# Performance work log

Measured on AMD Instinct MI355X. Metric: run time of the kernel, lower is better.

## Reference

```python
import jax, jax.numpy as jnp
import numpy as np

NALGOS = 64
NTASKS = 256
T = 4096  # len(lx)


def setup_inputs() -> dict:
    key = jax.random.key(0)
    ks = jax.random.split(key, 6)
    return {
        "lx": jax.random.randint(ks[0], (T,), 0, NTASKS),
        # task_matrix ~ U(-1, 1), as in the torch init
        "task_matrix": jax.random.uniform(ks[1], (NTASKS, NTASKS), jnp.float32) * 2.0 - 1.0,
        # task difficulty ~ U(0, 1); keep away from 0 to avoid division blowup
        "task_difficulty": jax.random.uniform(ks[2], (NTASKS,), jnp.float32, 0.05, 1.0),
        "alg_efficiency": 0.5 + 0.02 * jax.random.normal(ks[3], (NALGOS,), jnp.float32),
        "alg_memory_horizon": 0.5 + 0.1 * jax.random.normal(ks[4], (NALGOS,), jnp.float32),
        "alg_experience_boost": 0.5 + 0.02 * jax.random.normal(ks[5], (NALGOS,), jnp.float32),
    }


def reference(lx, task_matrix, task_difficulty, alg_efficiency,
              alg_memory_horizon, alg_experience_boost):
    # Faithful translation of IdealLearner.performance.
    # Original triple loop reads result[algo,task2,ind] and sig[algo,task,ind]
    # (previous timestep only) and writes index ind+1, so each timestep is
    # vectorizable over (algo, task2); only the time axis is a true recurrence.
    A = alg_efficiency.shape[0]
    N = task_matrix.shape[0]
    eff = alg_efficiency[:, None]        # (A,1)
    mem = alg_memory_horizon[:, None]    # (A,1)
    boost = alg_experience_boost[:, None]  # (A,1)
    diff = task_difficulty[None, :]      # (1,N) ; task_difficulty_scale == 1

    def step(carry, task):
        res_prev, sig_prev = carry              # each (A, N)
        tm = task_matrix[task][None, :]         # (1, N) row for current task
        sp = sig_prev[:, task][:, None]         # (A, 1) prior perf on current task
        res = res_prev * mem + tm * eff + tm * sp * boost
        sig = 2.0 * jax.nn.sigmoid(res / diff) - 1.0
        return (res, sig), sig

    z = jnp.zeros((A, N), task_matrix.dtype)
    _, ys = jax.lax.scan(step, (z, z), lx)      # ys: (T, A, N)
    # prepend the zero initial state -> (A, N, T+1), matching the torch output
    return jnp.concatenate([z[:, :, None], jnp.transpose(ys, (1, 2, 0))], axis=-1)
```

## Files before the change

kernel.cpp:

```cpp
#include <hip/hip_runtime.h>
#include <hip/hip_bf16.h>

#define NALGOS 64
#define NTASKS 256
#define TSTEPS 4096
#define CHUNK  256
#define NCHUNK (TSTEPS / CHUNK)
#define SUB    64
#define TP     257
#define LOG2E  1.44269504f

__global__ __launch_bounds__(64) void driver_kernel(
    const int* __restrict__ lx, const float* __restrict__ tmat,
    const float* __restrict__ diff, const float* __restrict__ eff_v,
    const float* __restrict__ mem_v, const float* __restrict__ boost_v,
    float* __restrict__ g_arr, float* __restrict__ ckpt) {
  __shared__ int    lx_s[TSTEPS + 8];
  __shared__ float  c_s[NTASKS];
  __shared__ float4 ctab[TSTEPS + 8];

  const int a = blockIdx.x;
  const int l = threadIdx.x;
  const float eff   = eff_v[a];
  const float mem   = mem_v[a];
  const float boost = boost_v[a];
  const float e0 = eff - boost;
  const float b2 = 2.0f * boost;

#pragma unroll 8
  for (int k = 0; k < TSTEPS / 64; ++k) lx_s[k * 64 + l] = lx[k * 64 + l];
  if (l < 8) lx_s[TSTEPS + l] = 0;
#pragma unroll
  for (int k = 0; k < NTASKS / 64; ++k) {
    float dk = diff[k * 64 + l];
    c_s[k * 64 + l] = -LOG2E / dk;
  }
  __syncthreads();

#pragma unroll 4
  for (int k = 0; k < TSTEPS / 64; ++k) {
    int i  = k * 64 + l;
    int t0 = lx_s[i];
    int t1 = (i + 1 < TSTEPS) ? lx_s[i + 1] : 0;
    int t2 = (i + 2 < TSTEPS) ? lx_s[i + 2] : 0;
    float q  = tmat[t0 * NTASKS + t1];
    float cp = c_s[t1];
    float4 e;
    e.x = cp;
    e.y = b2 * cp * q;
    e.z = e0 * cp * q;
    e.w = __int_as_float(t0 | (t2 << 16));
    ctab[i] = e;
  }
  if (l < 8) ctab[TSTEPS + l] = make_float4(0.f, 0.f, 0.f, __int_as_float(0));
  __syncthreads();

  const float4* rows = (const float4*)tmat;
  float* gout = g_arr + (size_t)a * TSTEPS;
  float* ck   = ckpt  + (size_t)a * NCHUNK * NTASKS;

  float r0 = 0.f, r1 = 0.f, r2 = 0.f, r3 = 0.f;
  float u = 2.0f;
  float keep_g = 0.f;

  float4 ct_cur = ctab[0];
  float4 ct_n1  = ctab[1];
  float4 ct_n2  = ctab[2];
  float  A = ct_cur.z;

  float4 tm0 = rows[lx_s[0] * 64 + l];
  float4 tm1 = rows[lx_s[1] * 64 + l];
  float4 tm2 = rows[lx_s[2] * 64 + l];
  float4 tm3 = rows[lx_s[3] * 64 + l];

#pragma unroll 4
  for (int t = 0; t < TSTEPS; ++t) {
    float w   = __builtin_amdgcn_rcpf(u);
    float g   = fmaf(b2, w, e0);
    float arg = fmaf(ct_cur.y, w, A);
    float ev  = __builtin_amdgcn_exp2f(arg);
    u = 1.0f + ev;

    keep_g = ((t & 63) == l) ? g : keep_g;

    r0 = fmaf(r0, mem, tm0.x * g);
    r1 = fmaf(r1, mem, tm0.y * g);
    r2 = fmaf(r2, mem, tm0.z * g);
    r3 = fmaf(r3, mem, tm0.w * g);

    int sb   = __float_as_int(ct_cur.w);
    int j2   = (sb >> 16) & 0xffff;
    int lane = j2 >> 2;
    float h01  = (j2 & 1) ? r1 : r0;
    float h23  = (j2 & 1) ? r3 : r2;
    float hsel = (j2 & 2) ? h23 : h01;
    float bro = __uint_as_float(
        __builtin_amdgcn_readlane(__float_as_uint(hsel), lane));
    float p = mem * bro;
    A = fmaf(ct_n1.x, p, ct_n1.z);

    ct_cur = ct_n1; ct_n1 = ct_n2; ct_n2 = ctab[t + 3];
    int nrow = lx_s[t + 4];
    tm0 = tm1; tm1 = tm2; tm2 = tm3;
    tm3 = rows[nrow * 64 + l];

    if ((t & 63) == 63) gout[t - 63 + l] = keep_g;
    if ((t & 255) == 255 && t < TSTEPS - 1) {
      float4 s; s.x = r0; s.y = r1; s.z = r2; s.w = r3;
      ((float4*)(ck + ((t + 1) >> 8) * NTASKS))[l] = s;
    }
  }
}

__global__ __launch_bounds__(256) void expand_kernel(
    const int* __restrict__ lx, const float* __restrict__ tmat,
    const float* __restrict__ diff, const float* __restrict__ mem_v,
    const float* __restrict__ g_arr, const float* __restrict__ ckpt,
    float* __restrict__ out) {
  __shared__ float tile[SUB * TP];
  __shared__ int   lx_c[CHUNK];
  __shared__ float g_c[CHUNK];

  const int c = blockIdx.x;
  const int a = blockIdx.y;
  const int n = threadIdx.x;

  const float mem = mem_v[a];
  const float cn  = -LOG2E / diff[n];
  float res = (c == 0) ? 0.f : ckpt[((size_t)a * NCHUNK + c) * NTASKS + n];

  const int t0 = c * CHUNK;
  lx_c[n] = lx[t0 + n];
  g_c[n]  = g_arr[(size_t)a * TSTEPS + t0 + n];
  __syncthreads();

  if (c == 0) out[((size_t)a * NTASKS + n) * (TSTEPS + 1)] = 0.f;

  const int tq   = threadIdx.x & 15;
  const int rloc = threadIdx.x >> 4;

  for (int tb = 0; tb < CHUNK; tb += SUB) {
#pragma unroll 8
    for (int ts = 0; ts < SUB; ++ts) {
      int   task = lx_c[tb + ts];
      float g    = g_c[tb + ts];
      float tm   = tmat[task * NTASKS + n];
      res = fmaf(res, mem, tm * g);
      float w = __builtin_amdgcn_rcpf(
          1.0f + __builtin_amdgcn_exp2f(cn * res));
      tile[ts * TP + n] = fmaf(2.0f, w, -1.0f);
    }
    __syncthreads();
    for (int rr = 0; rr < NTASKS; rr += 16) {
      const int row = rr + rloc;
      float v0 = tile[(4 * tq + 0) * TP + row];
      float v1 = tile[(4 * tq + 1) * TP + row];
      float v2 = tile[(4 * tq + 2) * TP + row];
      float v3 = tile[(4 * tq + 3) * TP + row];
      float4 v = make_float4(v0, v1, v2, v3);
      float* dst = &out[((size_t)a * NTASKS + row) * (TSTEPS + 1) +
                        t0 + tb + 4 * tq + 1];
      __builtin_memcpy(dst, &v, 16);
    }
    __syncthreads();
  }
}

extern "C" void kernel_launch(void* const* d_in, const int* in_sizes, int n_in,
                              void* d_out, int out_size, void* d_ws, size_t ws_size,
                              hipStream_t stream) {
  const int*   lx    = (const int*)d_in[0];
  const float* tmat  = (const float*)d_in[1];
  const float* diff  = (const float*)d_in[2];
  const float* eff   = (const float*)d_in[3];
  const float* mem   = (const float*)d_in[4];
  const float* boost = (const float*)d_in[5];
  float* out = (float*)d_out;

  float* g_arr = (float*)d_ws;
  float* ckpt  = g_arr + (size_t)NALGOS * TSTEPS;

  driver_kernel<<<NALGOS, 64, 0, stream>>>(lx, tmat, diff, eff, mem, boost,
                                           g_arr, ckpt);
  expand_kernel<<<dim3(NCHUNK, NALGOS), 256, 0, stream>>>(
      lx, tmat, diff, mem, g_arr, ckpt, out);
}
```

Before: 727.7 us.

## Deepen driver prefetch pipeline with register rings and remap expand grid

The driver kernel's serial recurrence loop now works in 64-step groups with a fully unrolled 32-step inner loop. It keeps a 4-deep ring of step coefficients and an 8-deep ring of task-matrix rows in registers, so row loads are issued 8 steps ahead instead of 4. The packed lane index and prefetch row are made wave-uniform via readfirstlane, and the per-step modulo checks for g and checkpoint stores are hoisted out to group boundaries. The expand kernel moves to a 1D grid with a custom block-to-(chunk, algo) mapping, probably to change how output writes are spread across memory channels. The cost is more registers held in the driver and a larger unrolled loop body.

```diff
diff --git a/kernel.cpp b/kernel.cpp
--- a/kernel.cpp
+++ b/kernel.cpp
@@ -15,7 +15,7 @@
     const float* __restrict__ diff, const float* __restrict__ eff_v,
     const float* __restrict__ mem_v, const float* __restrict__ boost_v,
     float* __restrict__ g_arr, float* __restrict__ ckpt) {
-  __shared__ int    lx_s[TSTEPS + 8];
+  __shared__ int    lx_s[TSTEPS + 16];
   __shared__ float  c_s[NTASKS];
   __shared__ float4 ctab[TSTEPS + 8];
 
@@ -29,7 +29,7 @@
 
 #pragma unroll 8
   for (int k = 0; k < TSTEPS / 64; ++k) lx_s[k * 64 + l] = lx[k * 64 + l];
-  if (l < 8) lx_s[TSTEPS + l] = 0;
+  if (l < 16) lx_s[TSTEPS + l] = 0;
 #pragma unroll
   for (int k = 0; k < NTASKS / 64; ++k) {
     float dk = diff[k * 64 + l];
@@ -41,15 +41,14 @@
   for (int k = 0; k < TSTEPS / 64; ++k) {
     int i  = k * 64 + l;
     int t0 = lx_s[i];
-    int t1 = (i + 1 < TSTEPS) ? lx_s[i + 1] : 0;
-    int t2 = (i + 2 < TSTEPS) ? lx_s[i + 2] : 0;
+    int t1 = lx_s[i + 1];
     float q  = tmat[t0 * NTASKS + t1];
     float cp = c_s[t1];
     float4 e;
     e.x = cp;
     e.y = b2 * cp * q;
     e.z = e0 * cp * q;
-    e.w = __int_as_float(t0 | (t2 << 16));
+    e.w = __int_as_float(lx_s[i + 2] | (lx_s[i + 8] << 16));
     ctab[i] = e;
   }
   if (l < 8) ctab[TSTEPS + l] = make_float4(0.f, 0.f, 0.f, __int_as_float(0));
@@ -63,51 +62,59 @@
   float u = 2.0f;
   float keep_g = 0.f;
 
-  float4 ct_cur = ctab[0];
-  float4 ct_n1  = ctab[1];
-  float4 ct_n2  = ctab[2];
-  float  A = ct_cur.z;
+  float4 ctr[4];
+  float4 tmr[8];
+#pragma unroll
+  for (int k = 0; k < 4; ++k) ctr[k] = ctab[k];
+#pragma unroll
+  for (int k = 0; k < 8; ++k) tmr[k] = rows[lx_s[k] * 64 + l];
+  float A = ctr[0].z;
 
-  float4 tm0 = rows[lx_s[0] * 64 + l];
-  float4 tm1 = rows[lx_s[1] * 64 + l];
-  float4 tm2 = rows[lx_s[2] * 64 + l];
-  float4 tm3 = rows[lx_s[3] * 64 + l];
+  for (int grp = 0; grp < TSTEPS / 64; ++grp) {
+#pragma unroll 1
+    for (int k32 = 0; k32 < 2; ++k32) {
+      const float4* cb = ctab + grp * 64 + k32 * 32;
+      const int kb = k32 * 32;
+#pragma unroll
+      for (int kk = 0; kk < 32; ++kk) {
+        const int k = kb + kk;
+        const float4 ct  = ctr[k & 3];
+        const float4 ctn = ctr[(k + 1) & 3];
+        const float4 tm  = tmr[k & 7];
 
-#pragma unroll 4
-  for (int t = 0; t < TSTEPS; ++t) {
-    float w   = __builtin_amdgcn_rcpf(u);
-    float g   = fmaf(b2, w, e0);
-    float arg = fmaf(ct_cur.y, w, A);
-    float ev  = __builtin_amdgcn_exp2f(arg);
-    u = 1.0f + ev;
+        float w   = __builtin_amdgcn_rcpf(u);
+        float gt  = fmaf(b2, w, e0);
+        float arg = fmaf(ct.y, w, A);
+        float ev  = __builtin_amdgcn_exp2f(arg);
+        u = 1.0f + ev;
 
-    keep_g = ((t & 63) == l) ? g : keep_g;
+        keep_g = (k == l) ? gt : keep_g;
 
-    r0 = fmaf(r0, mem, tm0.x * g);
-    r1 = fmaf(r1, mem, tm0.y * g);
-    r2 = fmaf(r2, mem, tm0.z * g);
-    r3 = fmaf(r3, mem, tm0.w * g);
+        r0 = fmaf(r0, mem, tm.x * gt);
+        r1 = fmaf(r1, mem, tm.y * gt);
+        r2 = fmaf(r2, mem, tm.z * gt);
+        r3 = fmaf(r3, mem, tm.w * gt);
 
-    int sb   = __float_as_int(ct_cur.w);
-    int j2   = (sb >> 16) & 0xffff;
-    int lane = j2 >> 2;
-    float h01  = (j2 & 1) ? r1 : r0;
-    float h23  = (j2 & 1) ? r3 : r2;
-    float hsel = (j2 & 2) ? h23 : h01;
-    float bro = __uint_as_float(
-        __builtin_amdgcn_readlane(__float_as_uint(hsel), lane));
-    float p = mem * bro;
-    A = fmaf(ct_n1.x, p, ct_n1.z);
+        const int sw   = __builtin_amdgcn_readfirstlane(__float_as_int(ct.w));
+        const int j2   = sw & 0xff;
+        const int lane = j2 >> 2;
+        float h01  = (j2 & 1) ? r1 : r0;
+        float h23  = (j2 & 1) ? r3 : r2;
+        float hsel = (j2 & 2) ? h23 : h01;
+        float bro = __uint_as_float(
+            __builtin_amdgcn_readlane(__float_as_uint(hsel), lane));
+        float p = mem * bro;
+        A = fmaf(ctn.x, p, ctn.z);
 
-    ct_cur = ct_n1; ct_n1 = ct_n2; ct_n2 = ctab[t + 3];
-    int nrow = lx_s[t + 4];
-    tm0 = tm1; tm1 = tm2; tm2 = tm3;
-    tm3 = rows[nrow * 64 + l];
-
-    if ((t & 63) == 63) gout[t - 63 + l] = keep_g;
-    if ((t & 255) == 255 && t < TSTEPS - 1) {
+        ctr[k & 3] = cb[kk + 4];
+        const int nrow = (sw >> 16) & 0xff;
+        tmr[k & 7] = rows[nrow * 64 + l];
+      }
+    }
+    gout[grp * 64 + l] = keep_g;
+    if ((grp & 3) == 3 && grp != 63) {
       float4 s; s.x = r0; s.y = r1; s.z = r2; s.w = r3;
-      ((float4*)(ck + ((t + 1) >> 8) * NTASKS))[l] = s;
+      ((float4*)(ck + ((grp + 1) >> 2) * NTASKS))[l] = s;
     }
   }
 }
@@ -121,9 +128,10 @@
   __shared__ int   lx_c[CHUNK];
   __shared__ float g_c[CHUNK];
 
-  const int c = blockIdx.x;
-  const int a = blockIdx.y;
-  const int n = threadIdx.x;
+  const int id = blockIdx.x;
+  const int c  = (id >> 3) & 15;
+  const int a  = (id & 7) + 8 * (id >> 7);
+  const int n  = threadIdx.x;
 
   const float mem = mem_v[a];
   const float cn  = -LOG2E / diff[n];
@@ -182,6 +190,6 @@
 
   driver_kernel<<<NALGOS, 64, 0, stream>>>(lx, tmat, diff, eff, mem, boost,
                                            g_arr, ckpt);
-  expand_kernel<<<dim3(NCHUNK, NALGOS), 256, 0, stream>>>(
+  expand_kernel<<<dim3(NCHUNK * NALGOS), 256, 0, stream>>>(
       lx, tmat, diff, mem, g_arr, ckpt, out);
 }
```

Measured after the change: 611.5 us. 16.0% less time.
